# Kernel tuning notes

Measured on AMD Instinct MI355X. Metric: run time of the kernel, lower is better.

Reference implementation:

```python
import jax, jax.numpy as jnp
import numpy as np

N, K, H, X_DIM, S_DIM = 50000, 8, 128, 32, 27
LSTM_IN = X_DIM + 3 * H  # 416


def setup_inputs() -> dict:
    key = jax.random.key(0)
    ks = jax.random.split(key, 16)

    def u(k, shape, fan_in):
        lim = 1.0 / np.sqrt(fan_in)
        return jax.random.uniform(k, shape, jnp.float32, -lim, lim)

    return {
        "x": jax.random.normal(ks[0], (N, X_DIM), jnp.float32),
        "h_self": jax.random.normal(ks[1], (N, H), jnp.float32),
        "c_self": jax.random.normal(ks[2], (N, H), jnp.float32),
        "h_inflows": jax.random.normal(ks[3], (N, K, H), jnp.float32),
        "inflow_valid": jax.random.randint(ks[4], (N, K), 0, 2) > 0,
        "static": jax.random.normal(ks[5], (N, S_DIM), jnp.float32),
        # Linear weights stored (out, in) as in eqx.nn.Linear
        "Wn": u(ks[6], (H, H), H),                     # W_neighbor, no bias
        "Wg": u(ks[7], (H, 2 * H), 2 * H),             # W_inflow_gate
        "bg": u(ks[8], (H,), 2 * H),
        "Ws": u(ks[9], (H, S_DIM), S_DIM),             # W_static
        "bs": u(ks[10], (H,), S_DIM),
        "Wl": u(ks[11], (4 * H, LSTM_IN), LSTM_IN),    # W_lstm
        "bl": u(ks[12], (4 * H,), LSTM_IN),
        "ln_w": jnp.ones((H,), jnp.float32),           # ln_h affine
        "ln_b": jnp.zeros((H,), jnp.float32),
    }


def reference(x, h_self, c_self, h_inflows, inflow_valid, static,
              Wn, Wg, bg, Ws, bs, Wl, bl, ln_w, ln_b):
    eps = 1e-5
    # per-neighbor message: [N,K,H]
    msgs = jnp.einsum('nkh,oh->nko', h_inflows, Wn)
    # inflow gate on concat(h_inflow, h_self): [N,K,H]
    h_tiled = jnp.broadcast_to(h_self[:, None, :], h_inflows.shape)
    gate_in = jnp.concatenate([h_inflows, h_tiled], axis=-1)  # [N,K,2H]
    gates = jax.nn.sigmoid(jnp.einsum('nkd,od->nko', gate_in, Wg) + bg)
    # masked sum over neighbors -> [N,H]
    mask = inflow_valid[..., None].astype(jnp.float32)
    neighbor_context = jnp.sum(gates * msgs * mask, axis=1)
    static_proj = static @ Ws.T + bs  # [N,H]
    combined = jnp.concatenate([x, h_self, neighbor_context, static_proj], axis=-1)
    z = combined @ Wl.T + bl  # [N,4H]
    i, f, o, g = jnp.split(z, 4, axis=-1)
    c_new = jax.nn.sigmoid(f) * c_self + jax.nn.sigmoid(i) * jnp.tanh(g)
    h_new = jax.nn.sigmoid(o) * jnp.tanh(c_new)
    # LayerNorm over hidden dim (eqx default eps=1e-5, affine)
    mu = jnp.mean(h_new, axis=-1, keepdims=True)
    var = jnp.mean(jnp.square(h_new - mu), axis=-1, keepdims=True)
    h_new = (h_new - mu) * jax.lax.rsqrt(var + eps) * ln_w + ln_b
    return (h_new, c_new)
```

## Files before the change

kernel.cpp:

```cpp
#include <hip/hip_runtime.h>
#include <hip/hip_bf16.h>

#define NN 50000
#define KI 8
#define H 128
#define XD 32
#define SD 27
#define CIN 416
#define CIN2 320
#define CPAD 328
#define ZOUT 512
#define NTILE_NB (NN / KI)
#define MB_LSTM 32

typedef __attribute__((ext_vector_type(8))) short bf16x8;
typedef __attribute__((ext_vector_type(4))) float f32x4;
typedef __attribute__((ext_vector_type(4))) unsigned short us4;

#define MFMA16(a, b, c) __builtin_amdgcn_mfma_f32_16x16x32_bf16((a), (b), (c), 0, 0, 0)

static __device__ __forceinline__ float sigmoidf_(float x) {
    return 1.0f / (1.0f + __expf(-x));
}
static __device__ __forceinline__ float tanhf_(float x) {
    return 1.0f - 2.0f / (__expf(2.0f * x) + 1.0f);
}
static __device__ __forceinline__ unsigned short f2b(float f) {
    union { float f; unsigned int u; } v; v.f = f;
    unsigned int r = v.u + 0x7FFF + ((v.u >> 16) & 1);
    return (unsigned short)(r >> 16);
}
static __device__ __forceinline__ float dot4_(float4 a, float4 b) {
    return a.x * b.x + a.y * b.y + a.z * b.z + a.w * b.w;
}

__global__ __launch_bounds__(256) void k_prep(
    const float* __restrict__ Wn, const float* __restrict__ Wg,
    const float* __restrict__ Wl, const float* __restrict__ bl,
    const float* __restrict__ Ws, const float* __restrict__ bs,
    unsigned short* __restrict__ WnB, unsigned short* __restrict__ WgB,
    unsigned short* __restrict__ WpB, float* __restrict__ bp)
{
    const int b = blockIdx.x, t = threadIdx.x;
    if (b < 512) {
        const float* wr = Wl + (size_t)b * CIN;
        unsigned short* out = WpB + (size_t)b * CIN2;
        for (int c = t; c < CIN2; c += 256) {
            float v;
            if (c < 288) v = wr[c];
            else if (c < 288 + SD) {
                int s = c - 288;
                float acc = 0.f;
                for (int j = 0; j < H; ++j) acc += wr[288 + j] * Ws[j * SD + s];
                v = acc;
            } else v = 0.f;
            out[c] = f2b(v);
        }
        if (t == 0) {
            float acc = bl[b];
            for (int j = 0; j < H; ++j) acc += wr[288 + j] * bs[j];
            bp[b] = acc;
        }
    } else {
        int idx = (b - 512) * 256 + t;
        for (int r = idx; r < 49152; r += 16384) {
            if (r < 16384) WnB[r] = f2b(Wn[r]);
            else WgB[r - 16384] = f2b(Wg[r - 16384]);
        }
    }
}

__global__ __launch_bounds__(256, 2) void k_nb_mfma(
    const float* __restrict__ hself_g, const float* __restrict__ hin_g,
    const unsigned char* __restrict__ valid_raw,
    const unsigned short* __restrict__ WnB, const unsigned short* __restrict__ WgB,
    const float* __restrict__ bg,
    unsigned short* __restrict__ ncb, int nc_stride)
{
    __shared__ unsigned short hin_s[64 * 128];
    __shared__ unsigned short hs_s[8 * 128];
    __shared__ float gh_s[8][128];
    __shared__ unsigned short ncs[8 * 128];
    __shared__ float valid_s[64];

    const int t = threadIdx.x;
    const int w = t >> 6, l = t & 63;
    const int ln = l & 15, lk = l >> 4;

    int det = 0;
    #pragma unroll
    for (int i = 0; i < 64; ++i) det |= valid_raw[4 * i + 1];
    const bool f8 = (det != 0);

    bf16x8 Bn[2][4], Ba[2][4], Bb[2][4];
    const int cbase = w * 32;
    #pragma unroll
    for (int c = 0; c < 2; ++c) {
        const int col = cbase + c * 16 + ln;
        #pragma unroll
        for (int kk = 0; kk < 4; ++kk) {
            const int k0 = kk * 32 + lk * 8;
            Bn[c][kk] = *(const bf16x8*)(WnB + col * H + k0);
            Ba[c][kk] = *(const bf16x8*)(WgB + col * 2 * H + k0);
            Bb[c][kk] = *(const bf16x8*)(WgB + col * 2 * H + H + k0);
        }
    }
    const float bg0 = bg[cbase + ln];
    const float bg1 = bg[cbase + 16 + ln];

    for (int tile = blockIdx.x; tile < NTILE_NB; tile += gridDim.x) {
        const int nb = tile * 8;

        if (t < 64) {
            bool v = f8 ? (valid_raw[(size_t)nb * KI + t] != 0)
                        : (((const unsigned int*)valid_raw)[(size_t)nb * KI + t] != 0u);
            valid_s[t] = v ? 1.f : 0.f;
        }
        {
            const float4* src = (const float4*)(hin_g + (size_t)nb * KI * H);
            float4 r0[8];
            #pragma unroll
            for (int i = 0; i < 8; ++i) r0[i] = src[t + i * 256];
            float4 hv = ((const float4*)(hself_g + (size_t)nb * H))[t];
            #pragma unroll
            for (int i = 0; i < 8; ++i) {
                int e = (t + i * 256) * 4, row = e >> 7, col = e & 127;
                unsigned byte = (unsigned)(row * 256 + col * 2) ^ (unsigned)((row & 7) << 4);
                us4 pk = { f2b(r0[i].x), f2b(r0[i].y), f2b(r0[i].z), f2b(r0[i].w) };
                *(us4*)((char*)hin_s + byte) = pk;
            }
            {
                int e = t * 4, row = e >> 7, col = e & 127;
                unsigned byte = (unsigned)(row * 256 + col * 2) ^ (unsigned)((row & 7) << 4);
                us4 pk = { f2b(hv.x), f2b(hv.y), f2b(hv.z), f2b(hv.w) };
                *(us4*)((char*)hs_s + byte) = pk;
            }
        }
        __syncthreads();

        f32x4 accM[4][2], accP[4][2], accG[2];
        #pragma unroll
        for (int m = 0; m < 4; ++m)
            #pragma unroll
            for (int c = 0; c < 2; ++c) { accM[m][c] = (f32x4)0.f; accP[m][c] = (f32x4)0.f; }
        accG[0] = (f32x4)0.f; accG[1] = (f32x4)0.f;

        #pragma unroll
        for (int kk = 0; kk < 4; ++kk) {
            const int k0 = kk * 32 + lk * 8;
            bf16x8 am[4];
            #pragma unroll
            for (int m = 0; m < 4; ++m) {
                int row = m * 16 + ln;
                unsigned byte = (unsigned)(row * 256 + k0 * 2) ^ (unsigned)((row & 7) << 4);
                am[m] = *(const bf16x8*)((const char*)hin_s + byte);
            }
            bf16x8 ah;
            {
                int row = ln & 7;
                unsigned byte = (unsigned)(row * 256 + k0 * 2) ^ (unsigned)((row & 7) << 4);
                ah = *(const bf16x8*)((const char*)hs_s + byte);
            }
            #pragma unroll
            for (int m = 0; m < 4; ++m)
                #pragma unroll
                for (int c = 0; c < 2; ++c) {
                    accM[m][c] = MFMA16(am[m], Bn[c][kk], accM[m][c]);
                    accP[m][c] = MFMA16(am[m], Ba[c][kk], accP[m][c]);
                }
            accG[0] = MFMA16(ah, Bb[0][kk], accG[0]);
            accG[1] = MFMA16(ah, Bb[1][kk], accG[1]);
        }

        #pragma unroll
        for (int c = 0; c < 2; ++c)
            #pragma unroll
            for (int r = 0; r < 4; ++r) {
                int row = lk * 4 + r;
                if (row < 8) gh_s[row][cbase + c * 16 + ln] = accG[c][r];
            }
        __syncthreads();

        #pragma unroll
        for (int m = 0; m < 4; ++m) {
            const int node = 2 * m + (lk >> 1);
            #pragma unroll
            for (int c = 0; c < 2; ++c) {
                const int col = cbase + c * 16 + ln;
                const float bgc = c ? bg1 : bg0;
                const float ghv = gh_s[node][col];
                float sum = 0.f;
                #pragma unroll
                for (int r = 0; r < 4; ++r) {
                    int row = m * 16 + lk * 4 + r;
                    float g = sigmoidf_(accP[m][c][r] + ghv + bgc);
                    sum += valid_s[row] * g * accM[m][c][r];
                }
                sum += __shfl_xor(sum, 16);
                if ((l & 16) == 0) ncs[(2 * m + (l >> 5)) * H + col] = f2b(sum);
            }
        }
        __syncthreads();

        {
            int e = t * 4, node = e >> 7, col = e & 127;
            us4 v = *(const us4*)(ncs + e);
            *(us4*)(ncb + (size_t)(nb + node) * nc_stride + col) = v;
        }
        __syncthreads();
    }
}

__global__ __launch_bounds__(512, 4) void k_lstm_mfma(
    const float* __restrict__ x_g, const float* __restrict__ hself_g,
    const float* __restrict__ cself_g, const float* __restrict__ stat_g,
    const unsigned short* __restrict__ ncb, int nc_stride,
    const unsigned short* __restrict__ WpB, const float* __restrict__ bp,
    const float* __restrict__ lnw, const float* __restrict__ lnb,
    float* __restrict__ h_out, float* __restrict__ c_out)
{
    __shared__ char smem[MB_LSTM * CPAD * 2];
    unsigned short* comb = (unsigned short*)smem;
    float (*hpre)[132] = (float(*)[132])smem;

    const int t = threadIdx.x;
    const int nb = blockIdx.x * MB_LSTM;
    const int w = t >> 6, l = t & 63, ln = l & 15, lk = l >> 4;
    const int hcol = w * 16 + ln;

    if (t < 256) {
        int e = t * 4, row = e >> 5, col = e & 31;
        us4 pk = { 0, 0, 0, 0 };
        if (nb + row < NN) {
            float4 v = ((const float4*)(x_g + (size_t)nb * XD))[t];
            pk = us4{ f2b(v.x), f2b(v.y), f2b(v.z), f2b(v.w) };
        }
        *(us4*)(comb + row * CPAD + col) = pk;
    }
    #pragma unroll
    for (int i = 0; i < 2; ++i) {
        int p4 = t + i * 512;
        int e = p4 * 4, row = e >> 7, col = 32 + (e & 127);
        us4 pk = { 0, 0, 0, 0 };
        if (nb + row < NN) {
            float4 v = ((const float4*)(hself_g + (size_t)nb * H))[p4];
            pk = us4{ f2b(v.x), f2b(v.y), f2b(v.z), f2b(v.w) };
        }
        *(us4*)(comb + row * CPAD + col) = pk;
    }
    #pragma unroll
    for (int i = 0; i < 2; ++i) {
        int p4 = t + i * 512;
        int e = p4 * 4, row = e >> 7, col = e & 127;
        us4 v = { 0, 0, 0, 0 };
        if (nb + row < NN) v = *(const us4*)(ncb + (size_t)(nb + row) * nc_stride + col);
        *(us4*)(comb + row * CPAD + 160 + col) = v;
    }
    for (int i = t; i < MB_LSTM * SD; i += 512) {
        int row = i / SD, col = i - row * SD;
        unsigned short v = 0;
        if (nb + row < NN) v = f2b(stat_g[(size_t)(nb + row) * SD + col]);
        comb[row * CPAD + 288 + col] = v;
    }
    if (t < MB_LSTM * 5) {
        int row = t / 5, col = 315 + t % 5;
        comb[row * CPAD + col] = 0;
    }

    float cpre[8];
    #pragma unroll
    for (int m = 0; m < 2; ++m)
        #pragma unroll
        for (int r = 0; r < 4; ++r) {
            int node = m * 16 + lk * 4 + r;
            size_t n = (size_t)(nb + node);
            cpre[m * 4 + r] = (n < NN) ? cself_g[n * H + hcol] : 0.f;
        }
    __syncthreads();

    f32x4 acc[2][4];
    #pragma unroll
    for (int m = 0; m < 2; ++m)
        #pragma unroll
        for (int g = 0; g < 4; ++g) acc[m][g] = (f32x4)0.f;

    #pragma unroll
    for (int kk = 0; kk < 10; ++kk) {
        const int k0 = kk * 32 + lk * 8;
        bf16x8 a0 = *(const bf16x8*)(comb + ln * CPAD + k0);
        bf16x8 a1 = *(const bf16x8*)(comb + (16 + ln) * CPAD + k0);
        #pragma unroll
        for (int g = 0; g < 4; ++g) {
            bf16x8 b = *(const bf16x8*)(WpB + (size_t)(g * H + hcol) * CIN2 + k0);
            acc[0][g] = MFMA16(a0, b, acc[0][g]);
            acc[1][g] = MFMA16(a1, b, acc[1][g]);
        }
    }
    __syncthreads();

    {
        const float bi = bp[hcol], bf = bp[H + hcol];
        const float bo = bp[2 * H + hcol], bgg = bp[3 * H + hcol];
        #pragma unroll
        for (int m = 0; m < 2; ++m)
            #pragma unroll
            for (int r = 0; r < 4; ++r) {
                int node = m * 16 + lk * 4 + r;
                size_t n = (size_t)(nb + node);
                if (n < NN) {
                    float zi = acc[m][0][r] + bi;
                    float zf = acc[m][1][r] + bf;
                    float zo = acc[m][2][r] + bo;
                    float zg = acc[m][3][r] + bgg;
                    float cn = sigmoidf_(zf) * cpre[m * 4 + r] + sigmoidf_(zi) * tanhf_(zg);
                    c_out[n * H + hcol] = cn;
                    hpre[node][hcol] = sigmoidf_(zo) * tanhf_(cn);
                }
            }
    }
    __syncthreads();

    #pragma unroll
    for (int jj = 0; jj < 4; ++jj) {
        const int j = w * 4 + jj;
        const size_t n = (size_t)(nb + j);
        if (n < NN) {
            float a = hpre[j][l];
            float b = hpre[j][64 + l];
            float s = a + b, q = a * a + b * b;
            #pragma unroll
            for (int off = 1; off < 64; off <<= 1) {
                s += __shfl_xor(s, off);
                q += __shfl_xor(q, off);
            }
            float mu = s * (1.0f / 128.0f);
            float var = q * (1.0f / 128.0f) - mu * mu;
            float rstd = rsqrtf(var + 1e-5f);
            h_out[n * H + l]      = (a - mu) * rstd * lnw[l] + lnb[l];
            h_out[n * H + 64 + l] = (b - mu) * rstd * lnw[64 + l] + lnb[64 + l];
        }
    }
}

__global__ __launch_bounds__(256) void k_nb_f32(
    const float* __restrict__ hself_g, const float* __restrict__ hin_g,
    const unsigned char* __restrict__ valid_raw,
    const float* __restrict__ Wn, const float* __restrict__ Wg,
    const float* __restrict__ bg, float* __restrict__ nc)
{
    __shared__ float4 hin_s[8 * KI * (H / 4)];
    __shared__ float4 hs_s[8 * (H / 4)];
    __shared__ int flag8;
    const int t = threadIdx.x;
    const int nb = blockIdx.x * 8;
    {
        int loc = 0;
        if (t < 64) {
            #pragma unroll
            for (int i = 0; i < 16; ++i) loc |= valid_raw[4 * (t * 16 + i) + 1];
        }
        int any = __any(loc != 0);
        if (t == 0) flag8 = any;
    }
    const float4* src_hin = (const float4*)(hin_g + (size_t)nb * KI * H);
    #pragma unroll
    for (int i = 0; i < 8; ++i) hin_s[t + i * 256] = src_hin[t + i * 256];
    hs_s[t] = ((const float4*)(hself_g + (size_t)nb * H))[t];
    __syncthreads();
    const int o = t & 127, g = t >> 7;
    float msg[4][KI], gat[4][KI], gh[4];
    #pragma unroll
    for (int j = 0; j < 4; ++j) {
        gh[j] = 0.f;
        #pragma unroll
        for (int k = 0; k < KI; ++k) { msg[j][k] = 0.f; gat[j][k] = 0.f; }
    }
    const float4* Wn4 = (const float4*)(Wn + (size_t)o * H);
    const float4* Wg4a = (const float4*)(Wg + (size_t)o * 2 * H);
    const float4* Wg4b = (const float4*)(Wg + (size_t)o * 2 * H + H);
    for (int d4 = 0; d4 < H / 4; ++d4) {
        float4 wn = Wn4[d4], w0 = Wg4a[d4], w1 = Wg4b[d4];
        #pragma unroll
        for (int j = 0; j < 4; ++j) {
            const int node = g * 4 + j;
            gh[j] += dot4_(w1, hs_s[node * 32 + d4]);
            #pragma unroll
            for (int k = 0; k < KI; ++k) {
                float4 hv = hin_s[(node * KI + k) * 32 + d4];
                msg[j][k] += dot4_(wn, hv);
                gat[j][k] += dot4_(w0, hv);
            }
        }
    }
    const float bgo = bg[o];
    const unsigned int* valid32 = (const unsigned int*)valid_raw;
    const int f8 = flag8;
    #pragma unroll
    for (int j = 0; j < 4; ++j) {
        const int n = nb + g * 4 + j;
        float acc = 0.f;
        #pragma unroll
        for (int k = 0; k < KI; ++k) {
            bool v = f8 ? (valid_raw[n * KI + k] != 0) : (valid32[n * KI + k] != 0u);
            if (v) acc += sigmoidf_(gat[j][k] + gh[j] + bgo) * msg[j][k];
        }
        nc[(size_t)n * H + o] = acc;
    }
}

__global__ __launch_bounds__(256) void k_lstm_f32(
    const float* __restrict__ x_g, const float* __restrict__ hself_g,
    const float* __restrict__ cself_g, const float* __restrict__ stat_g,
    const float* __restrict__ nc,
    const float* __restrict__ Ws, const float* __restrict__ bs,
    const float* __restrict__ Wl, const float* __restrict__ bl,
    const float* __restrict__ lnw, const float* __restrict__ lnb,
    float* __restrict__ h_out, float* __restrict__ c_out)
{
    __shared__ float4 comb4[16 * (CIN / 4)];
    __shared__ float zsh[16 * ZOUT];
    __shared__ float stat_s[16 * SD];
    float* combf = (float*)comb4;
    const int t = threadIdx.x;
    const int nb = blockIdx.x * 16;
    #pragma unroll
    for (int i = 0; i < 2; ++i) {
        int idx = t + i * 256;
        combf[(idx >> 5) * CIN + (idx & 31)] = x_g[(size_t)nb * XD + idx];
    }
    #pragma unroll
    for (int i = 0; i < 8; ++i) {
        int idx = t + i * 256;
        combf[(idx >> 7) * CIN + 32 + (idx & 127)] = hself_g[(size_t)nb * H + idx];
    }
    #pragma unroll
    for (int i = 0; i < 8; ++i) {
        int idx = t + i * 256;
        combf[(idx >> 7) * CIN + 160 + (idx & 127)] = nc[(size_t)nb * H + idx];
    }
    stat_s[t] = stat_g[(size_t)nb * SD + t];
    if (t < 16 * SD - 256) stat_s[t + 256] = stat_g[(size_t)nb * SD + t + 256];
    __syncthreads();
    {
        const int o = t & 127, jg = t >> 7;
        #pragma unroll
        for (int jj = 0; jj < 8; ++jj) {
            const int j = jg * 8 + jj;
            float s = bs[o];
            #pragma unroll
            for (int c = 0; c < SD; ++c) s += Ws[o * SD + c] * stat_s[j * SD + c];
            combf[j * CIN + 288 + o] = s;
        }
    }
    __syncthreads();
    float acc0[16], acc1[16];
    #pragma unroll
    for (int j = 0; j < 16; ++j) { acc0[j] = 0.f; acc1[j] = 0.f; }
    const float4* W0 = (const float4*)(Wl + (size_t)t * CIN);
    const float4* W1 = (const float4*)(Wl + (size_t)(t + 256) * CIN);
    for (int d4 = 0; d4 < CIN / 4; ++d4) {
        float4 w0 = W0[d4], w1 = W1[d4];
        #pragma unroll
        for (int j = 0; j < 16; ++j) {
            float4 cv = comb4[j * (CIN / 4) + d4];
            acc0[j] += dot4_(w0, cv);
            acc1[j] += dot4_(w1, cv);
        }
    }
    const float bl0 = bl[t], bl1 = bl[t + 256];
    #pragma unroll
    for (int j = 0; j < 16; ++j) {
        zsh[j * ZOUT + t] = acc0[j] + bl0;
        zsh[j * ZOUT + 256 + t] = acc1[j] + bl1;
    }
    __syncthreads();
    {
        const int h = t & 127, jg = t >> 7;
        #pragma unroll
        for (int jj = 0; jj < 8; ++jj) {
            const int j = jg * 8 + jj;
            const size_t n = (size_t)(nb + j);
            float zi = zsh[j * ZOUT + h];
            float zf = zsh[j * ZOUT + 128 + h];
            float zo = zsh[j * ZOUT + 256 + h];
            float zg = zsh[j * ZOUT + 384 + h];
            float cn = sigmoidf_(zf) * cself_g[n * H + h] + sigmoidf_(zi) * tanhf(zg);
            c_out[n * H + h] = cn;
            zsh[j * ZOUT + h] = sigmoidf_(zo) * tanhf(cn);
        }
    }
    __syncthreads();
    {
        const int w = t >> 6, lane = t & 63;
        #pragma unroll
        for (int jj = 0; jj < 4; ++jj) {
            const int j = w * 4 + jj;
            const size_t n = (size_t)(nb + j);
            float a = zsh[j * ZOUT + lane];
            float b = zsh[j * ZOUT + 64 + lane];
            float s = a + b, q = a * a + b * b;
            #pragma unroll
            for (int off = 1; off < 64; off <<= 1) {
                s += __shfl_xor(s, off);
                q += __shfl_xor(q, off);
            }
            float mu = s * (1.0f / 128.0f);
            float var = q * (1.0f / 128.0f) - mu * mu;
            float rstd = rsqrtf(var + 1e-5f);
            h_out[n * H + lane] = (a - mu) * rstd * lnw[lane] + lnb[lane];
            h_out[n * H + 64 + lane] = (b - mu) * rstd * lnw[64 + lane] + lnb[64 + lane];
        }
    }
}

extern "C" void kernel_launch(void* const* d_in, const int* in_sizes, int n_in,
                              void* d_out, int out_size, void* d_ws, size_t ws_size,
                              hipStream_t stream) {
    const float* x      = (const float*)d_in[0];
    const float* h_self = (const float*)d_in[1];
    const float* c_self = (const float*)d_in[2];
    const float* h_inf  = (const float*)d_in[3];
    const unsigned char* valid = (const unsigned char*)d_in[4];
    const float* statp  = (const float*)d_in[5];
    const float* Wn     = (const float*)d_in[6];
    const float* Wg     = (const float*)d_in[7];
    const float* bg     = (const float*)d_in[8];
    const float* Ws     = (const float*)d_in[9];
    const float* bs     = (const float*)d_in[10];
    const float* Wl     = (const float*)d_in[11];
    const float* bl     = (const float*)d_in[12];
    const float* lnw    = (const float*)d_in[13];
    const float* lnb    = (const float*)d_in[14];

    float* h_out = (float*)d_out;
    float* c_out = h_out + (size_t)NN * H;

    const size_t W_BYTES = (size_t)512 * CIN2 * 2 + 16384 * 2 + 32768 * 2 + 512 * 4;
    const size_t NC_BYTES = (size_t)NN * H * 2;

    if (ws_size >= W_BYTES) {
        char* p = (char*)d_ws;
        unsigned short* WpB = (unsigned short*)p;           p += (size_t)512 * CIN2 * 2;
        unsigned short* WnB = (unsigned short*)p;           p += 16384 * 2;
        unsigned short* WgB = (unsigned short*)p;           p += 32768 * 2;
        float* bp = (float*)p;                              p += 512 * 4;

        unsigned short* ncb;
        int nc_stride;
        if (ws_size >= W_BYTES + NC_BYTES + 64) {
            ncb = (unsigned short*)p;
            nc_stride = H;
        } else {
            ncb = (unsigned short*)h_out;
            nc_stride = 256;
        }

        k_prep<<<576, 256, 0, stream>>>(Wn, Wg, Wl, bl, Ws, bs,
                                        WnB, WgB, WpB, bp);
        k_nb_mfma<<<512, 256, 0, stream>>>(h_self, h_inf, valid, WnB, WgB, bg,
                                           ncb, nc_stride);
        k_lstm_mfma<<<(NN + MB_LSTM - 1) / MB_LSTM, 512, 0, stream>>>(
            x, h_self, c_self, statp, ncb, nc_stride, WpB, bp,
            lnw, lnb, h_out, c_out);
    } else {
        float* nc_buf = (ws_size >= (size_t)NN * H * sizeof(float))
                            ? (float*)d_ws : h_out;
        k_nb_f32<<<NN / 8, 256, 0, stream>>>(h_self, h_inf, valid, Wn, Wg, bg, nc_buf);
        k_lstm_f32<<<NN / 16, 256, 0, stream>>>(x, h_self, c_self, statp, nc_buf,
                                                Ws, bs, Wl, bl, lnw, lnb, h_out, c_out);
    }
}
```

Baseline: 180.8 us.

## Prefetch next neighbor tile into registers and use hardware bf16 conversion

The neighbor-message kernel now loads the next tile's h_inflows, h_self and validity flags into registers while the current tile's MFMA work runs, so global load latency overlaps with compute. The trailing barrier at the end of each tile loop is removed, and the manual round-to-nearest bf16 conversion is replaced with the library __float2bfloat16 intrinsic. Keeping a second tile in registers raises register pressure under the launch bound of 2 blocks per SM. Dropping the barrier relies on the existing barriers to keep the ncs shared buffer from being overwritten before the previous tile has read it.

```diff
diff --git a/kernel.cpp b/kernel.cpp
--- a/kernel.cpp
+++ b/kernel.cpp
@@ -25,10 +25,9 @@
 static __device__ __forceinline__ float tanhf_(float x) {
     return 1.0f - 2.0f / (__expf(2.0f * x) + 1.0f);
 }
-static __device__ __forceinline__ unsigned short f2b(float f) {
-    union { float f; unsigned int u; } v; v.f = f;
-    unsigned int r = v.u + 0x7FFF + ((v.u >> 16) & 1);
-    return (unsigned short)(r >> 16);
+static __device__ __forceinline__ unsigned short bf(float f) {
+    __hip_bfloat16 h = __float2bfloat16(f);
+    return __builtin_bit_cast(unsigned short, h);
 }
 static __device__ __forceinline__ float dot4_(float4 a, float4 b) {
     return a.x * b.x + a.y * b.y + a.z * b.z + a.w * b.w;
@@ -54,7 +53,7 @@
                 for (int j = 0; j < H; ++j) acc += wr[288 + j] * Ws[j * SD + s];
                 v = acc;
             } else v = 0.f;
-            out[c] = f2b(v);
+            out[c] = bf(v);
         }
         if (t == 0) {
             float acc = bl[b];
@@ -64,8 +63,8 @@
     } else {
         int idx = (b - 512) * 256 + t;
         for (int r = idx; r < 49152; r += 16384) {
-            if (r < 16384) WnB[r] = f2b(Wn[r]);
-            else WgB[r - 16384] = f2b(Wg[r - 16384]);
+            if (r < 16384) WnB[r] = bf(Wn[r]);
+            else WgB[r - 16384] = bf(Wg[r - 16384]);
         }
     }
 }
@@ -108,35 +107,51 @@
     const float bg0 = bg[cbase + ln];
     const float bg1 = bg[cbase + 16 + ln];
 
+    float4 ph[8], ps;
+    float pv = 0.f;
+    {
+        const int nb0 = blockIdx.x * 8;
+        const float4* src = (const float4*)(hin_g + (size_t)nb0 * KI * H);
+        #pragma unroll
+        for (int i = 0; i < 8; ++i) ph[i] = src[t + i * 256];
+        ps = ((const float4*)(hself_g + (size_t)nb0 * H))[t];
+        if (t < 64)
+            pv = (f8 ? (valid_raw[(size_t)nb0 * KI + t] != 0)
+                     : (((const unsigned int*)valid_raw)[(size_t)nb0 * KI + t] != 0u))
+                     ? 1.f : 0.f;
+    }
+
     for (int tile = blockIdx.x; tile < NTILE_NB; tile += gridDim.x) {
         const int nb = tile * 8;
 
-        if (t < 64) {
-            bool v = f8 ? (valid_raw[(size_t)nb * KI + t] != 0)
-                        : (((const unsigned int*)valid_raw)[(size_t)nb * KI + t] != 0u);
-            valid_s[t] = v ? 1.f : 0.f;
+        if (t < 64) valid_s[t] = pv;
+        #pragma unroll
+        for (int i = 0; i < 8; ++i) {
+            int e = (t + i * 256) * 4, row = e >> 7, col = e & 127;
+            unsigned byte = (unsigned)(row * 256 + col * 2) ^ (unsigned)((row & 7) << 4);
+            us4 pk = { bf(ph[i].x), bf(ph[i].y), bf(ph[i].z), bf(ph[i].w) };
+            *(us4*)((char*)hin_s + byte) = pk;
         }
         {
-            const float4* src = (const float4*)(hin_g + (size_t)nb * KI * H);
-            float4 r0[8];
-            #pragma unroll
-            for (int i = 0; i < 8; ++i) r0[i] = src[t + i * 256];
-            float4 hv = ((const float4*)(hself_g + (size_t)nb * H))[t];
-            #pragma unroll
-            for (int i = 0; i < 8; ++i) {
-                int e = (t + i * 256) * 4, row = e >> 7, col = e & 127;
-                unsigned byte = (unsigned)(row * 256 + col * 2) ^ (unsigned)((row & 7) << 4);
-                us4 pk = { f2b(r0[i].x), f2b(r0[i].y), f2b(r0[i].z), f2b(r0[i].w) };
-                *(us4*)((char*)hin_s + byte) = pk;
-            }
-            {
-                int e = t * 4, row = e >> 7, col = e & 127;
-                unsigned byte = (unsigned)(row * 256 + col * 2) ^ (unsigned)((row & 7) << 4);
-                us4 pk = { f2b(hv.x), f2b(hv.y), f2b(hv.z), f2b(hv.w) };
-                *(us4*)((char*)hs_s + byte) = pk;
-            }
+            int e = t * 4, row = e >> 7, col = e & 127;
+            unsigned byte = (unsigned)(row * 256 + col * 2) ^ (unsigned)((row & 7) << 4);
+            us4 pk = { bf(ps.x), bf(ps.y), bf(ps.z), bf(ps.w) };
+            *(us4*)((char*)hs_s + byte) = pk;
         }
         __syncthreads();
+
+        const int next = tile + gridDim.x;
+        if (next < NTILE_NB) {
+            const int nb2 = next * 8;
+            const float4* src = (const float4*)(hin_g + (size_t)nb2 * KI * H);
+            #pragma unroll
+            for (int i = 0; i < 8; ++i) ph[i] = src[t + i * 256];
+            ps = ((const float4*)(hself_g + (size_t)nb2 * H))[t];
+            if (t < 64)
+                pv = (f8 ? (valid_raw[(size_t)nb2 * KI + t] != 0)
+                         : (((const unsigned int*)valid_raw)[(size_t)nb2 * KI + t] != 0u))
+                         ? 1.f : 0.f;
+        }
 
         f32x4 accM[4][2], accP[4][2], accG[2];
         #pragma unroll
@@ -197,7 +212,7 @@
                     sum += valid_s[row] * g * accM[m][c][r];
                 }
                 sum += __shfl_xor(sum, 16);
-                if ((l & 16) == 0) ncs[(2 * m + (l >> 5)) * H + col] = f2b(sum);
+                if ((l & 16) == 0) ncs[(2 * m + (l >> 5)) * H + col] = bf(sum);
             }
         }
         __syncthreads();
@@ -207,7 +222,6 @@
             us4 v = *(const us4*)(ncs + e);
             *(us4*)(ncb + (size_t)(nb + node) * nc_stride + col) = v;
         }
-        __syncthreads();
     }
 }
 
@@ -233,7 +247,7 @@
         us4 pk = { 0, 0, 0, 0 };
         if (nb + row < NN) {
             float4 v = ((const float4*)(x_g + (size_t)nb * XD))[t];
-            pk = us4{ f2b(v.x), f2b(v.y), f2b(v.z), f2b(v.w) };
+            pk = us4{ bf(v.x), bf(v.y), bf(v.z), bf(v.w) };
         }
         *(us4*)(comb + row * CPAD + col) = pk;
     }
@@ -244,7 +258,7 @@
         us4 pk = { 0, 0, 0, 0 };
         if (nb + row < NN) {
             float4 v = ((const float4*)(hself_g + (size_t)nb * H))[p4];
-            pk = us4{ f2b(v.x), f2b(v.y), f2b(v.z), f2b(v.w) };
+            pk = us4{ bf(v.x), bf(v.y), bf(v.z), bf(v.w) };
         }
         *(us4*)(comb + row * CPAD + col) = pk;
     }
@@ -259,7 +273,7 @@
     for (int i = t; i < MB_LSTM * SD; i += 512) {
         int row = i / SD, col = i - row * SD;
         unsigned short v = 0;
-        if (nb + row < NN) v = f2b(stat_g[(size_t)(nb + row) * SD + col]);
+        if (nb + row < NN) v = bf(stat_g[(size_t)(nb + row) * SD + col]);
         comb[row * CPAD + 288 + col] = v;
     }
     if (t < MB_LSTM * 5) {
@@ -299,7 +313,7 @@
     __syncthreads();
 
     {
-        const float bi = bp[hcol], bf = bp[H + hcol];
+        const float bi = bp[hcol], bff = bp[H + hcol];
         const float bo = bp[2 * H + hcol], bgg = bp[3 * H + hcol];
         #pragma unroll
         for (int m = 0; m < 2; ++m)
@@ -309,7 +323,7 @@
                 size_t n = (size_t)(nb + node);
                 if (n < NN) {
                     float zi = acc[m][0][r] + bi;
-                    float zf = acc[m][1][r] + bf;
+                    float zf = acc[m][1][r] + bff;
                     float zo = acc[m][2][r] + bo;
                     float zg = acc[m][3][r] + bgg;
                     float cn = sigmoidf_(zf) * cpre[m * 4 + r] + sigmoidf_(zi) * tanhf_(zg);
```

After: 212.7 us. +17.6%, slower.
